# Optimization experiments

Hardware: AMD Instinct MI355X
Metric: run time of the kernel (lower is better)

The kernel has to match this reference:

```python
import jax, jax.numpy as jnp
import numpy as np

N = 8  # block_size

def _dct_matrix(n):
    m = np.zeros((n, n), dtype=np.float32)
    for k in range(n):
        for t in range(n):
            if k == 0:
                m[k, t] = np.sqrt(1.0 / n)
            else:
                m[k, t] = np.sqrt(2.0 / n) * np.cos(np.pi * k * (2 * t + 1) / (2 * n))
    return m

def _zigzag(n):
    idxs = np.zeros((n, n), dtype=np.int64)
    idx = 0
    for s in range(2 * n - 1):
        if s % 2 == 0:
            rng = range(min(s, n - 1), max(0, s - n + 1) - 1, -1)
        else:
            rng = range(max(0, s - n + 1), min(s, n - 1) + 1)
        for i in rng:
            j = s - i
            if 0 <= i < n and 0 <= j < n:
                idxs[i, j] = idx
                idx += 1
    return idxs

def _band_masks(n):
    zz = _zigzag(n)
    total = n * n
    lo_t, hi_t = total // 3, 2 * total // 3
    low = (zz < lo_t).astype(np.float32)
    mid = ((zz >= lo_t) & (zz < hi_t)).astype(np.float32)
    high = (zz >= hi_t).astype(np.float32)
    return low, mid, high

_D = jnp.asarray(_dct_matrix(N))
_LOW, _MID, _HIGH = (jnp.asarray(m) for m in _band_masks(N))

def setup_inputs() -> dict:
    key = jax.random.key(0)
    x = jax.random.normal(key, (16, 3, 512, 512), dtype=jnp.float32)
    band_scale = jnp.ones((3,), dtype=jnp.float32)
    return {"x": x, "band_scale": band_scale}

def reference(x, band_scale):
    B, C, H, W = x.shape
    pad_h = (N - H % N) % N
    pad_w = (N - W % N) % N
    if pad_h > 0 or pad_w > 0:
        x = jnp.pad(x, ((0, 0), (0, 0), (0, pad_h), (0, pad_w)), mode="reflect")
    Hp, Wp = x.shape[2], x.shape[3]
    nH, nW = Hp // N, Wp // N
    # [B,C,nH,N,nW,N] -> blocks [B,C,nH,nW,N,N]
    blocks = x.reshape(B, C, nH, N, nW, N).transpose(0, 1, 2, 4, 3, 5)
    # 2D DCT-II: D @ X @ D^T
    coeffs = jnp.einsum("km,bchwmn,ln->bchwkl", _D, blocks, _D)

    def idct_band(mask, scale):
        c = coeffs * mask
        # IDCT: D^T @ C @ D
        sp = jnp.einsum("km,bchwkl,ln->bchwmn", _D, c, _D)
        out = sp.transpose(0, 1, 2, 4, 3, 5).reshape(B, C, Hp, Wp)
        return out[:, :, :H, :W] * scale

    low = idct_band(_LOW, band_scale[0])
    mid = idct_band(_MID, band_scale[1])
    high = idct_band(_HIGH, band_scale[2])
    return (low, mid, high)
```

## Files before the change

### kernel.cpp

```cpp
#include <hip/hip_runtime.h>

#define IMG   512
#define NIMG  48
#define PLANE (IMG * IMG)
#define OUTCH ((size_t)NIMG * PLANE)
#define NTHREADS (NIMG * 64 * 64)

__device__ constexpr float Dm[8][8] = {
  { 0.3535533905932738f, 0.3535533905932738f, 0.3535533905932738f, 0.3535533905932738f,
    0.3535533905932738f, 0.3535533905932738f, 0.3535533905932738f, 0.3535533905932738f},
  { 0.4903926402016152f, 0.4157348061512726f, 0.2777851165098011f, 0.0975451610080642f,
   -0.0975451610080642f,-0.2777851165098011f,-0.4157348061512726f,-0.4903926402016152f},
  { 0.4619397662556434f, 0.1913417161825449f,-0.1913417161825449f,-0.4619397662556434f,
   -0.4619397662556434f,-0.1913417161825449f, 0.1913417161825449f, 0.4619397662556434f},
  { 0.4157348061512726f,-0.0975451610080642f,-0.4903926402016152f,-0.2777851165098011f,
    0.2777851165098011f, 0.4903926402016152f, 0.0975451610080642f,-0.4157348061512726f},
  { 0.3535533905932738f,-0.3535533905932738f,-0.3535533905932738f, 0.3535533905932738f,
    0.3535533905932738f,-0.3535533905932738f,-0.3535533905932738f, 0.3535533905932738f},
  { 0.2777851165098011f,-0.4903926402016152f, 0.0975451610080642f, 0.4157348061512726f,
   -0.4157348061512726f,-0.0975451610080642f, 0.4903926402016152f,-0.2777851165098011f},
  { 0.1913417161825449f,-0.4619397662556434f, 0.4619397662556434f,-0.1913417161825449f,
   -0.1913417161825449f, 0.4619397662556434f,-0.4619397662556434f, 0.1913417161825449f},
  { 0.0975451610080642f,-0.2777851165098011f, 0.4157348061512726f,-0.4903926402016152f,
    0.4903926402016152f,-0.4157348061512726f, 0.2777851165098011f,-0.0975451610080642f},
};

__device__ constexpr int ZZ[8][8] = {
  {  0,  1,  5,  6, 14, 15, 27, 28},
  {  2,  4,  7, 13, 16, 26, 29, 42},
  {  3,  8, 12, 17, 25, 30, 41, 43},
  {  9, 11, 18, 24, 31, 40, 44, 53},
  { 10, 19, 23, 32, 39, 45, 52, 54},
  { 20, 22, 33, 38, 46, 51, 55, 60},
  { 21, 34, 37, 47, 50, 56, 59, 61},
  { 35, 36, 48, 49, 57, 58, 62, 63},
};

template <int LO, int HI>
__device__ __forceinline__ void idct_band_store(const float A[8][8],
                                                float* __restrict__ dst,
                                                float scale) {
  float U[8][8];
#pragma unroll
  for (int l = 0; l < 8; ++l) {
#pragma unroll
    for (int m = 0; m < 8; ++m) {
      float acc = 0.0f;
#pragma unroll
      for (int k = 0; k < 8; ++k) {
        if (ZZ[k][l] >= LO && ZZ[k][l] < HI) acc += Dm[k][m] * A[k][l];
      }
      U[m][l] = acc;
    }
  }
#pragma unroll
  for (int m = 0; m < 8; ++m) {
    float t[8];
#pragma unroll
    for (int n = 0; n < 8; ++n) {
      float acc = 0.0f;
#pragma unroll
      for (int l = 0; l < 8; ++l) acc += U[m][l] * Dm[l][n];
      t[n] = acc * scale;
    }
    *(float4*)(dst + (size_t)m * IMG)     = make_float4(t[0], t[1], t[2], t[3]);
    *(float4*)(dst + (size_t)m * IMG + 4) = make_float4(t[4], t[5], t[6], t[7]);
  }
}

__global__ __launch_bounds__(256) void dct_decomp_kernel(
    const float* __restrict__ x, const float* __restrict__ band_scale,
    float* __restrict__ out) {
  int tid = blockIdx.x * 256 + threadIdx.x;
  if (tid >= NTHREADS) return;

  int bw  = tid & 63;
  int bh  = (tid >> 6) & 63;
  int img = tid >> 12;

  size_t base = ((size_t)img * IMG + (size_t)bh * 8) * IMG + (size_t)bw * 8;
  const float* src = x + base;

  float A[8][8];
#pragma unroll
  for (int r = 0; r < 8; ++r) {
    float4 v0 = *(const float4*)(src + (size_t)r * IMG);
    float4 v1 = *(const float4*)(src + (size_t)r * IMG + 4);
    A[r][0] = v0.x; A[r][1] = v0.y; A[r][2] = v0.z; A[r][3] = v0.w;
    A[r][4] = v1.x; A[r][5] = v1.y; A[r][6] = v1.z; A[r][7] = v1.w;
  }

#pragma unroll
  for (int m = 0; m < 8; ++m) {
    float t[8];
#pragma unroll
    for (int l = 0; l < 8; ++l) {
      float acc = 0.0f;
#pragma unroll
      for (int n = 0; n < 8; ++n) acc += A[m][n] * Dm[l][n];
      t[l] = acc;
    }
#pragma unroll
    for (int l = 0; l < 8; ++l) A[m][l] = t[l];
  }
#pragma unroll
  for (int l = 0; l < 8; ++l) {
    float t[8];
#pragma unroll
    for (int k = 0; k < 8; ++k) {
      float acc = 0.0f;
#pragma unroll
      for (int m = 0; m < 8; ++m) acc += Dm[k][m] * A[m][l];
      t[k] = acc;
    }
#pragma unroll
    for (int k = 0; k < 8; ++k) A[k][l] = t[k];
  }

  float s0 = band_scale[0];
  float s1 = band_scale[1];
  float s2 = band_scale[2];

  idct_band_store< 0, 21>(A, out + base,             s0);
  idct_band_store<21, 42>(A, out + OUTCH + base,     s1);
  idct_band_store<42, 64>(A, out + 2 * OUTCH + base, s2);
}

extern "C" void kernel_launch(void* const* d_in, const int* in_sizes, int n_in,
                              void* d_out, int out_size, void* d_ws, size_t ws_size,
                              hipStream_t stream) {
  const float* x          = (const float*)d_in[0];
  const float* band_scale = (const float*)d_in[1];
  float* out              = (float*)d_out;

  dim3 grid(NTHREADS / 256);
  dim3 block(256);
  dct_decomp_kernel<<<grid, block, 0, stream>>>(x, band_scale, out);
}
```

Before: 190.8 us.

## Split each 8x8 block across two lanes and derive high band by subtraction

Each 8x8 DCT block is now handled by a pair of lanes, each owning a 4-column half. The two lanes exchange partial transforms with __shfl_xor, which doubles thread count and cuts per-thread registers; launch bounds request 3 waves per SIMD. The high band is computed as input minus the low and mid reconstructions instead of a third inverse DCT, which saves arithmetic. That relies on the orthogonal DCT reconstructing exactly and may change float rounding slightly.

Result: slower. 226.3 us (+18.6%).

```diff
diff --git a/kernel.cpp b/kernel.cpp
--- a/kernel.cpp
+++ b/kernel.cpp
@@ -1,10 +1,8 @@
 #include <hip/hip_runtime.h>
 
-#define IMG   512
-#define NIMG  48
-#define PLANE (IMG * IMG)
-#define OUTCH ((size_t)NIMG * PLANE)
-#define NTHREADS (NIMG * 64 * 64)
+#define IMG 512
+#define OUTCH ((size_t)48 * 512 * 512)
+#define NTHREADS (48 * 64 * 128)
 
 __device__ constexpr float Dm[8][8] = {
   { 0.3535533905932738f, 0.3535533905932738f, 0.3535533905932738f, 0.3535533905932738f,
@@ -36,94 +34,142 @@
   { 35, 36, 48, 49, 57, 58, 62, 63},
 };
 
-template <int LO, int HI>
-__device__ __forceinline__ void idct_band_store(const float A[8][8],
-                                                float* __restrict__ dst,
-                                                float scale) {
-  float U[8][8];
+template <int L0>
+__device__ __forceinline__ void horiz_fwd(const float (&T)[8][4],
+                                          const float (&To)[8][4],
+                                          float (&C)[8][4]) {
 #pragma unroll
-  for (int l = 0; l < 8; ++l) {
+  for (int k = 0; k < 8; ++k) {
+    float F[8];
 #pragma unroll
-    for (int m = 0; m < 8; ++m) {
+    for (int j = 0; j < 4; ++j) {
+      F[(L0 == 0) ? j     : 4 + j] = T[k][j];
+      F[(L0 == 0) ? 4 + j : j    ] = To[k][j];
+    }
+#pragma unroll
+    for (int j = 0; j < 4; ++j) {
       float acc = 0.0f;
 #pragma unroll
-      for (int k = 0; k < 8; ++k) {
-        if (ZZ[k][l] >= LO && ZZ[k][l] < HI) acc += Dm[k][m] * A[k][l];
-      }
-      U[m][l] = acc;
+      for (int n = 0; n < 8; ++n) acc += F[n] * Dm[L0 + j][n];
+      C[k][j] = acc;
     }
-  }
-#pragma unroll
-  for (int m = 0; m < 8; ++m) {
-    float t[8];
-#pragma unroll
-    for (int n = 0; n < 8; ++n) {
-      float acc = 0.0f;
-#pragma unroll
-      for (int l = 0; l < 8; ++l) acc += U[m][l] * Dm[l][n];
-      t[n] = acc * scale;
-    }
-    *(float4*)(dst + (size_t)m * IMG)     = make_float4(t[0], t[1], t[2], t[3]);
-    *(float4*)(dst + (size_t)m * IMG + 4) = make_float4(t[4], t[5], t[6], t[7]);
   }
 }
 
-__global__ __launch_bounds__(256) void dct_decomp_kernel(
+template <int L0, int LOB, int HIB>
+__device__ __forceinline__ void stage1(const float (&C)[8][4], float (&U)[8][4]) {
+#pragma unroll
+  for (int m = 0; m < 8; ++m)
+#pragma unroll
+    for (int j = 0; j < 4; ++j) {
+      float acc = 0.0f;
+#pragma unroll
+      for (int k = 0; k < 8; ++k)
+        if (ZZ[k][L0 + j] >= LOB && ZZ[k][L0 + j] < HIB) acc += Dm[k][m] * C[k][j];
+      U[m][j] = acc;
+    }
+}
+
+template <int L0>
+__device__ __forceinline__ void stage2(const float (&U)[8][4],
+                                       const float (&Uo)[8][4],
+                                       float (&V)[8][4]) {
+#pragma unroll
+  for (int m = 0; m < 8; ++m) {
+    float F[8];
+#pragma unroll
+    for (int j = 0; j < 4; ++j) {
+      F[(L0 == 0) ? j     : 4 + j] = U[m][j];
+      F[(L0 == 0) ? 4 + j : j    ] = Uo[m][j];
+    }
+#pragma unroll
+    for (int j = 0; j < 4; ++j) {
+      float acc = 0.0f;
+#pragma unroll
+      for (int l = 0; l < 8; ++l) acc += F[l] * Dm[l][L0 + j];
+      V[m][j] = acc;
+    }
+  }
+}
+
+__global__ __launch_bounds__(256, 3) void dct_decomp_kernel(
     const float* __restrict__ x, const float* __restrict__ band_scale,
     float* __restrict__ out) {
   int tid = blockIdx.x * 256 + threadIdx.x;
-  if (tid >= NTHREADS) return;
+  int pc  = tid & 127;
+  int bh  = (tid >> 7) & 63;
+  int img = tid >> 13;
+  bool odd = (pc & 1) != 0;
 
-  int bw  = tid & 63;
-  int bh  = (tid >> 6) & 63;
-  int img = tid >> 12;
-
-  size_t base = ((size_t)img * IMG + (size_t)bh * 8) * IMG + (size_t)bw * 8;
+  size_t base = ((size_t)img * IMG + (size_t)bh * 8) * IMG + (size_t)pc * 4;
   const float* src = x + base;
 
-  float A[8][8];
+  float X[8][4];
 #pragma unroll
   for (int r = 0; r < 8; ++r) {
-    float4 v0 = *(const float4*)(src + (size_t)r * IMG);
-    float4 v1 = *(const float4*)(src + (size_t)r * IMG + 4);
-    A[r][0] = v0.x; A[r][1] = v0.y; A[r][2] = v0.z; A[r][3] = v0.w;
-    A[r][4] = v1.x; A[r][5] = v1.y; A[r][6] = v1.z; A[r][7] = v1.w;
+    float4 v = *(const float4*)(src + (size_t)r * IMG);
+    X[r][0] = v.x; X[r][1] = v.y; X[r][2] = v.z; X[r][3] = v.w;
   }
 
+  float T[8][4];
 #pragma unroll
-  for (int m = 0; m < 8; ++m) {
-    float t[8];
+  for (int k = 0; k < 8; ++k)
 #pragma unroll
-    for (int l = 0; l < 8; ++l) {
+    for (int j = 0; j < 4; ++j) {
       float acc = 0.0f;
 #pragma unroll
-      for (int n = 0; n < 8; ++n) acc += A[m][n] * Dm[l][n];
-      t[l] = acc;
+      for (int r = 0; r < 8; ++r) acc += Dm[k][r] * X[r][j];
+      T[k][j] = acc;
     }
+
+  float To[8][4];
 #pragma unroll
-    for (int l = 0; l < 8; ++l) A[m][l] = t[l];
-  }
+  for (int k = 0; k < 8; ++k)
 #pragma unroll
-  for (int l = 0; l < 8; ++l) {
-    float t[8];
-#pragma unroll
-    for (int k = 0; k < 8; ++k) {
-      float acc = 0.0f;
-#pragma unroll
-      for (int m = 0; m < 8; ++m) acc += Dm[k][m] * A[m][l];
-      t[k] = acc;
-    }
-#pragma unroll
-    for (int k = 0; k < 8; ++k) A[k][l] = t[k];
-  }
+    for (int j = 0; j < 4; ++j) To[k][j] = __shfl_xor(T[k][j], 1);
+
+  float C[8][4];
+  if (!odd) horiz_fwd<0>(T, To, C); else horiz_fwd<4>(T, To, C);
 
   float s0 = band_scale[0];
   float s1 = band_scale[1];
   float s2 = band_scale[2];
 
-  idct_band_store< 0, 21>(A, out + base,             s0);
-  idct_band_store<21, 42>(A, out + OUTCH + base,     s1);
-  idct_band_store<42, 64>(A, out + 2 * OUTCH + base, s2);
+  float U[8][4], Uo[8][4], V[8][4];
+
+  if (!odd) stage1<0, 0, 21>(C, U); else stage1<4, 0, 21>(C, U);
+#pragma unroll
+  for (int m = 0; m < 8; ++m)
+#pragma unroll
+    for (int j = 0; j < 4; ++j) Uo[m][j] = __shfl_xor(U[m][j], 1);
+  if (!odd) stage2<0>(U, Uo, V); else stage2<4>(U, Uo, V);
+#pragma unroll
+  for (int m = 0; m < 8; ++m) {
+    float4 w = make_float4(V[m][0] * s0, V[m][1] * s0, V[m][2] * s0, V[m][3] * s0);
+    *(float4*)(out + base + (size_t)m * IMG) = w;
+#pragma unroll
+    for (int j = 0; j < 4; ++j) X[m][j] -= V[m][j];
+  }
+
+  if (!odd) stage1<0, 21, 42>(C, U); else stage1<4, 21, 42>(C, U);
+#pragma unroll
+  for (int m = 0; m < 8; ++m)
+#pragma unroll
+    for (int j = 0; j < 4; ++j) Uo[m][j] = __shfl_xor(U[m][j], 1);
+  if (!odd) stage2<0>(U, Uo, V); else stage2<4>(U, Uo, V);
+#pragma unroll
+  for (int m = 0; m < 8; ++m) {
+    float4 w = make_float4(V[m][0] * s1, V[m][1] * s1, V[m][2] * s1, V[m][3] * s1);
+    *(float4*)(out + OUTCH + base + (size_t)m * IMG) = w;
+#pragma unroll
+    for (int j = 0; j < 4; ++j) X[m][j] -= V[m][j];
+  }
+
+#pragma unroll
+  for (int m = 0; m < 8; ++m) {
+    float4 w = make_float4(X[m][0] * s2, X[m][1] * s2, X[m][2] * s2, X[m][3] * s2);
+    *(float4*)(out + 2 * OUTCH + base + (size_t)m * IMG) = w;
+  }
 }
 
 extern "C" void kernel_launch(void* const* d_in, const int* in_sizes, int n_in,
```
